# Performance work log

Hardware: AMD Instinct MI355X
Metric: run time of the kernel (lower is better)

## Reference

```python
import jax, jax.numpy as jnp
import numpy as np

GROUPS = 32
EPS = 1e-6

def groupnorm(x, gamma, beta):
    b, c, h, w = x.shape
    xg = x.reshape(b, GROUPS, c // GROUPS, h, w)
    mu = xg.mean(axis=(2, 3, 4), keepdims=True)
    var = xg.var(axis=(2, 3, 4), keepdims=True)
    xn = ((xg - mu) / jnp.sqrt(var + EPS)).reshape(b, c, h, w)
    return xn * gamma[None, :, None, None] + beta[None, :, None, None]

def conv1x1(x, w, b):
    return jnp.einsum('oc,bchw->bohw', w, x) + b[None, :, None, None]

def attn_branch(xn, wq, bq, wk, bk, v_flat, scale):
    q = conv1x1(xn, wq, bq)
    k = conv1x1(xn, wk, bk)
    b_, c, h, w = q.shape
    qf = q.reshape(b_, c, h * w)   # b c n
    kf = k.reshape(b_, c, h * w)   # b c n
    scores = jnp.einsum('bci,bcj->bij', qf, kf) * scale  # b n n
    attn = jax.nn.softmax(scores, axis=2)
    out = jnp.einsum('bcj,bij->bci', v_flat, attn)       # b c n
    return out.reshape(b_, c, h, w)

def setup_inputs() -> dict:
    key = jax.random.key(0)
    ks = jax.random.split(key, 14)
    B, C, H, W = 4, 64, 64, 64
    R = C // 16  # SE reduction
    s = 0.05
    return {
        'x1': jax.random.normal(ks[0], (B, C, H, W), jnp.float32),
        'x2': jax.random.normal(ks[1], (B, C, H, W), jnp.float32),
        'se_w1': jax.random.normal(ks[2], (R, C), jnp.float32) * s,
        'se_w2': jax.random.normal(ks[3], (C, R), jnp.float32) * s,
        'gn_gamma': jnp.ones((C,), jnp.float32),
        'gn_beta': jnp.zeros((C,), jnp.float32),
        'wq': jax.random.normal(ks[4], (C, C), jnp.float32) * s,
        'bq': jnp.zeros((C,), jnp.float32),
        'wk': jax.random.normal(ks[5], (C, C), jnp.float32) * s,
        'bk': jnp.zeros((C,), jnp.float32),
        'wv': jax.random.normal(ks[6], (C, C), jnp.float32) * s,
        'bv': jnp.zeros((C,), jnp.float32),
    }

def reference(x1, x2, se_w1, se_w2, gn_gamma, gn_beta, wq, bq, wk, bk, wv, bv):
    x = x1 + x2
    # SE channel attention (ends in sigmoid), then an EXTRA sigmoid as in source
    y = x.mean(axis=(2, 3))                         # b c
    y = jax.nn.relu(y @ se_w1.T)                    # b r
    y = jax.nn.sigmoid(y @ se_w2.T)                 # b c
    se = x * y[:, :, None, None]
    ch_w = jax.nn.sigmoid(se)
    xn = groupnorm(x, gn_gamma, gn_beta)
    v = conv1x1(xn, wv, bv)
    b_, c, h, w = v.shape
    v_flat = v.reshape(b_, c, h * w)
    scale = 1.0 / jnp.sqrt(jnp.float32(c))
    # source reuses q1/k1 convs for BOTH branches
    h1 = attn_branch(groupnorm(x1, gn_gamma, gn_beta), wq, bq, wk, bk, v_flat, scale)
    h2 = attn_branch(groupnorm(x2, gn_gamma, gn_beta), wq, bq, wk, bk, v_flat, scale)
    return 2.0 * h1 * ch_w + 2.0 * h2 * (1.0 - ch_w)
```

## Files before the change

kernel.cpp:

```cpp
#include <hip/hip_runtime.h>

#define STATS_OFF 0
#define AD_OFF    20480
#define SEY_OFF   26624
#define WQB_OFF   32768
#define WKB_OFF   40960
#define WVB_OFF   49152
#define Q_OFF     57344
#define K_OFF     (Q_OFF + 4194304)
#define V_OFF     (K_OFF + 4194304)
#define PO_OFF    (V_OFF + 2097152)

#define QSCALE 0.18033688f
#define SWZ(r) ((((r) & 7) << 3) ^ (((r) & 8) << 1))

typedef __attribute__((ext_vector_type(8))) short  short8;
typedef __attribute__((ext_vector_type(4))) short  s16x4;
typedef __attribute__((ext_vector_type(2))) unsigned int u32x2;
typedef __attribute__((ext_vector_type(4))) float  f32x4;

#if __has_builtin(__builtin_amdgcn_exp2f)
__device__ inline float fexp2(float x) { return __builtin_amdgcn_exp2f(x); }
#else
__device__ inline float fexp2(float x) { return exp2f(x); }
#endif

__device__ inline ushort f2b(float f) {
  return (ushort)((__float_as_uint(f) + 0x8000u) >> 16);
}
__device__ inline unsigned pack2(float x, float y) {
  unsigned ux = __float_as_uint(x) + 0x8000u;
  unsigned uy = __float_as_uint(y) + 0x8000u;
  return __builtin_amdgcn_perm(uy, ux, 0x07060302);
}
__device__ inline float b2f(ushort u) { return __uint_as_float(((unsigned)u) << 16); }

__device__ inline f32x4 mfma16(short8 a, short8 b, f32x4 c) {
  return __builtin_amdgcn_mfma_f32_16x16x32_bf16(a, b, c, 0, 0, 0);
}

__device__ inline float wsum64(float v) {
  #pragma unroll
  for (int o = 32; o > 0; o >>= 1) v += __shfl_down(v, o, 64);
  return v;
}

__global__ __launch_bounds__(256) void sc_stats(const float* __restrict__ x1,
                                                const float* __restrict__ x2,
                                                float* __restrict__ stats,
                                                const float* __restrict__ wq,
                                                const float* __restrict__ wk,
                                                const float* __restrict__ wv,
                                                ushort* __restrict__ wqb,
                                                ushort* __restrict__ wkb,
                                                ushort* __restrict__ wvb) {
  int blk = blockIdx.x;
  int bc = blk >> 2, chunk = blk & 3;
  const float4* p1 = (const float4*)(x1 + (size_t)bc * 4096 + chunk * 1024);
  const float4* p2 = (const float4*)(x2 + (size_t)bc * 4096 + chunk * 1024);
  float4 a = p1[threadIdx.x], b = p2[threadIdx.x];
  float s1 = a.x + a.y + a.z + a.w;
  float q1 = a.x*a.x + a.y*a.y + a.z*a.z + a.w*a.w;
  float s2 = b.x + b.y + b.z + b.w;
  float q2 = b.x*b.x + b.y*b.y + b.z*b.z + b.w*b.w;
  float p12 = a.x*b.x + a.y*b.y + a.z*b.z + a.w*b.w;
  s1 = wsum64(s1); q1 = wsum64(q1); s2 = wsum64(s2); q2 = wsum64(q2); p12 = wsum64(p12);
  __shared__ float red[4][5];
  int w = threadIdx.x >> 6, ln = threadIdx.x & 63;
  if (ln == 0) { red[w][0] = s1; red[w][1] = q1; red[w][2] = s2; red[w][3] = q2; red[w][4] = p12; }
  __syncthreads();
  if (threadIdx.x < 5) {
    float acc = 0;
    #pragma unroll
    for (int ww = 0; ww < 4; ww++) acc += red[ww][threadIdx.x];
    stats[(size_t)blk * 5 + threadIdx.x] = acc;
  }
  if (blk >= 976) {
    int idx = (blk - 976) * 256 + threadIdx.x;
    int arr = idx >> 12, e = idx & 4095;
    if (arr == 0)      wqb[e] = f2b(wq[e] * QSCALE);
    else if (arr == 1) wkb[e] = f2b(wk[e]);
    else               wvb[e] = f2b(wv[e]);
  }
}

__global__ __launch_bounds__(256) void sc_prep(const float* __restrict__ stats,
                                               const float* __restrict__ w1,
                                               const float* __restrict__ w2,
                                               const float* __restrict__ gamma,
                                               const float* __restrict__ beta,
                                               float* __restrict__ ad, float* __restrict__ sey) {
  int t = threadIdx.x; int b = t >> 6, c = t & 63;
  float s1 = 0, q1 = 0, s2 = 0, q2 = 0, p12 = 0;
  #pragma unroll
  for (int ch = 0; ch < 4; ch++) {
    const float* sp = stats + (size_t)(t * 4 + ch) * 5;
    s1 += sp[0]; q1 += sp[1]; s2 += sp[2]; q2 += sp[3]; p12 += sp[4];
  }
  float sx = s1 + s2, qx = q1 + q2 + 2.f * p12;
  __shared__ float smu[256], sS[3][256], sQ[3][256], sy[16];
  smu[t] = sx * (1.f / 4096.f);
  sS[0][t] = sx; sQ[0][t] = qx; sS[1][t] = s1; sQ[1][t] = q1; sS[2][t] = s2; sQ[2][t] = q2;
  __syncthreads();
  if (t < 16) {
    int bb = t >> 2, r = t & 3; float acc = 0.f;
    for (int cc = 0; cc < 64; cc++) acc += w1[r*64+cc] * smu[bb*64+cc];
    sy[t] = fmaxf(acc, 0.f);
  }
  __syncthreads();
  float acc = 0.f;
  #pragma unroll
  for (int r = 0; r < 4; r++) acc += w2[c*4+r] * sy[b*4+r];
  sey[t] = 1.f / (1.f + fexp2(-acc * 1.44269504f));
  int prt = t ^ 1;
  float g = gamma[c], bt = beta[c];
  #pragma unroll
  for (int s = 0; s < 3; s++) {
    float S = sS[s][t] + sS[s][prt], Q = sQ[s][t] + sQ[s][prt];
    float mean = S * (1.f / 8192.f);
    float var  = Q * (1.f / 8192.f) - mean * mean;
    float rstd = rsqrtf(var + 1e-6f);
    float a = g * rstd;
    ad[((s*256) + t)*2 + 0] = a;
    ad[((s*256) + t)*2 + 1] = bt - mean * a;
  }
}

__global__ __launch_bounds__(256) void sc_proj(const float* __restrict__ x1, const float* __restrict__ x2,
    const float* __restrict__ ad,
    const float* __restrict__ wq, const float* __restrict__ bq,
    const float* __restrict__ wk, const float* __restrict__ bk,
    const float* __restrict__ wv, const float* __restrict__ bv,
    const ushort* __restrict__ wqb, const ushort* __restrict__ wkb, const ushort* __restrict__ wvb,
    ushort* __restrict__ qout, ushort* __restrict__ kout, ushort* __restrict__ vout) {
  int pt = blockIdx.x, src = blockIdx.y, b = blockIdx.z, t = threadIdx.x;
  __shared__ ushort xlds[64 * 66];
  __shared__ ushort olds[64 * 66];
  __shared__ float sd[64], sbias[2][64];
  if (t < 64) sd[t] = ad[((src*256) + b*64 + t)*2 + 1];
  __syncthreads();
  {
    int c = t >> 2, pq = (t & 3) * 16;
    const float* px1 = x1 + ((size_t)(b*64 + c))*4096 + pt*64 + pq;
    const float* px2 = x2 + ((size_t)(b*64 + c))*4096 + pt*64 + pq;
    float av = ad[((src*256) + b*64 + c)*2 + 0];
    #pragma unroll
    for (int k4 = 0; k4 < 4; k4++) {
      float4 v1 = *(const float4*)(px1 + 4*k4);
      float xv[4];
      if (src == 1) { xv[0]=v1.x; xv[1]=v1.y; xv[2]=v1.z; xv[3]=v1.w; }
      else {
        float4 v2 = *(const float4*)(px2 + 4*k4);
        if (src == 2) { xv[0]=v2.x; xv[1]=v2.y; xv[2]=v2.z; xv[3]=v2.w; }
        else { xv[0]=v1.x+v2.x; xv[1]=v1.y+v2.y; xv[2]=v1.z+v2.z; xv[3]=v1.w+v2.w; }
      }
      #pragma unroll
      for (int k = 0; k < 4; k++)
        xlds[(pq + 4*k4 + k)*66 + c] = f2b(av * xv[k]);
    }
  }
  int nbias = (src == 0) ? 64 : 128;
  if (t < nbias) {
    int proj = t >> 6, o = t & 63;
    const float* W  = (src == 0) ? wv : (proj == 0 ? wq : wk);
    const float* bs = (src == 0) ? bv : (proj == 0 ? bq : bk);
    float acc = bs[o];
    for (int cc = 0; cc < 64; cc++) acc += W[o*64+cc] * sd[cc];
    if (src != 0 && proj == 0) acc *= QSCALE;
    sbias[proj][o] = acc;
  }
  __syncthreads();
  int wave = t >> 6, lane = t & 63, quad = lane >> 4, l15 = lane & 15;
  int orow = t >> 2, ocol = (t & 3) * 16;
  if (src == 0) {
    const ushort* ap = wvb + (wave*16 + l15)*64 + quad*8;
    short8 a0 = *(const short8*)ap;
    short8 a1 = *(const short8*)(ap + 32);
    f32x4 cinit;
    #pragma unroll
    for (int r = 0; r < 4; r++) cinit[r] = sbias[0][wave*16 + quad*4 + r];
    #pragma unroll
    for (int s = 0; s < 4; s++) {
      const ushort* bp = xlds + (s*16 + l15)*66 + quad*8;
      short8 b0 = *(const short8*)bp;
      short8 b1 = *(const short8*)(bp + 32);
      f32x4 acc = mfma16(a0, b0, cinit);
      acc = mfma16(a1, b1, acc);
      #pragma unroll
      for (int r = 0; r < 4; r++)
        olds[(wave*16 + quad*4 + r)*66 + s*16 + l15] = f2b(acc[r]);
    }
    __syncthreads();
    uint4 w0 = *(const uint4*)&olds[orow*66 + ocol];
    uint4 w1 = *(const uint4*)&olds[orow*66 + ocol + 8];
    ushort* dst = vout + ((size_t)(b*64 + orow))*4096 + pt*64 + ocol;
    *(uint4*)dst = w0; *(uint4*)(dst + 8) = w1;
  } else {
    int bh = b*2 + (src - 1);
    const ushort* ap = xlds + (wave*16 + l15)*66 + quad*8;
    short8 a0 = *(const short8*)ap;
    short8 a1 = *(const short8*)(ap + 32);
    #pragma unroll
    for (int proj = 0; proj < 2; proj++) {
      const ushort* Wb = proj == 0 ? wqb : wkb;
      ushort* dst = proj == 0 ? qout : kout;
      #pragma unroll
      for (int s = 0; s < 4; s++) {
        const ushort* bp = Wb + (s*16 + l15)*64 + quad*8;
        short8 b0 = *(const short8*)bp;
        short8 b1 = *(const short8*)(bp + 32);
        float bb = sbias[proj][s*16 + l15];
        f32x4 acc = {bb, bb, bb, bb};
        acc = mfma16(a0, b0, acc);
        acc = mfma16(a1, b1, acc);
        #pragma unroll
        for (int r = 0; r < 4; r++)
          olds[(wave*16 + quad*4 + r)*66 + s*16 + l15] = f2b(acc[r]);
      }
      __syncthreads();
      uint4 w0 = *(const uint4*)&olds[orow*66 + ocol];
      uint4 w1 = *(const uint4*)&olds[orow*66 + ocol + 8];
      ushort* dp = dst + ((size_t)bh*4096 + pt*64 + orow)*64 + ocol;
      *(uint4*)dp = w0; *(uint4*)(dp + 8) = w1;
      if (proj == 0) __syncthreads();
    }
  }
}

__global__ __launch_bounds__(256, 2) void sc_flash(const ushort* __restrict__ qg,
                                                   const ushort* __restrict__ kg,
                                                   const ushort* __restrict__ vg,
                                                   ushort* __restrict__ po,
                                                   float* __restrict__ pl,
                                                   int jsbits) {
  int blk = blockIdx.x;
  int bh = blk & 7, rest = blk >> 3;
  int njs = 1 << jsbits, njt = 64 >> jsbits;
  int js = rest & (njs - 1), itile = rest >> jsbits;
  int jbase = js * (njt << 6);
  int b = bh >> 1;
  int t = threadIdx.x, wave = t >> 6, lane = t & 63, quad = lane >> 4, l15 = lane & 15;
  int i0 = itile * 256 + wave * 64;

  __shared__ ushort Klds[64 * 64];
  __shared__ ushort Vlds[64 * 64];

  short8 Qb[4][2];
  #pragma unroll
  for (int ib = 0; ib < 4; ib++) {
    const ushort* qp = qg + ((size_t)bh * 4096 + i0 + ib * 16 + l15) * 64 + quad * 8;
    Qb[ib][0] = *(const short8*)qp;
    Qb[ib][1] = *(const short8*)(qp + 32);
  }

  f32x4 O[4][4]; const f32x4 zero4 = {0.f, 0.f, 0.f, 0.f};
  #pragma unroll
  for (int ib = 0; ib < 4; ib++)
    #pragma unroll
    for (int cb = 0; cb < 4; cb++) O[ib][cb] = zero4;
  float lsum[4] = {0.f, 0.f, 0.f, 0.f};

  int sr = t >> 2, sc = (t & 3) * 16;
  int swzs = SWZ(sr);
  int swzl = SWZ(l15);
  const ushort* ksrc = kg + ((size_t)bh * 4096 + jbase + sr) * 64 + sc;
  const ushort* vsrc = vg + ((size_t)(b * 64 + sr)) * 4096 + jbase + sc;
  ushort* kd0 = Klds + sr * 64 + (sc ^ swzs);
  ushort* kd1 = Klds + sr * 64 + ((sc + 8) ^ swzs);
  ushort* vd0 = Vlds + sr * 64 + (sc ^ swzs);
  ushort* vd1 = Vlds + sr * 64 + ((sc + 8) ^ swzs);

  uint4 kr0 = *(const uint4*)ksrc, kr1 = *(const uint4*)(ksrc + 8);
  uint4 vr0 = *(const uint4*)vsrc, vr1 = *(const uint4*)(vsrc + 8);
  ksrc += 4096; vsrc += 64;

  #pragma unroll 1
  for (int jt = 0; jt < njt; jt++) {
    __syncthreads();
    *(uint4*)kd0 = kr0; *(uint4*)kd1 = kr1;
    *(uint4*)vd0 = vr0; *(uint4*)vd1 = vr1;
    __syncthreads();
    if (jt + 1 < njt) {
      kr0 = *(const uint4*)ksrc; kr1 = *(const uint4*)(ksrc + 8);
      vr0 = *(const uint4*)vsrc; vr1 = *(const uint4*)(vsrc + 8);
      ksrc += 4096; vsrc += 64;
    }

    #pragma unroll
    for (int s = 0; s < 4; s++) {
      int rowK = (s * 16 + l15) * 64;
      short8 ka0 = *(const short8*)&Klds[rowK + ((quad * 8) ^ swzl)];
      short8 ka1 = *(const short8*)&Klds[rowK + ((quad * 8 + 32) ^ swzl)];
      f32x4 S[4];
      #pragma unroll
      for (int ib = 0; ib < 4; ib++) {
        f32x4 acc = mfma16(ka0, Qb[ib][0], zero4);
        S[ib] = mfma16(ka1, Qb[ib][1], acc);
      }
      s16x4 vbf[4];
      #pragma unroll
      for (int cb = 0; cb < 4; cb++)
        vbf[cb] = *(const s16x4*)&Vlds[(cb * 16 + l15) * 64 + ((s * 16 + quad * 4) ^ swzl)];
      #pragma unroll
      for (int ib = 0; ib < 4; ib++) {
        float p0 = fexp2(S[ib][0]);
        float p1 = fexp2(S[ib][1]);
        float p2 = fexp2(S[ib][2]);
        float p3 = fexp2(S[ib][3]);
        lsum[ib] += (p0 + p1) + (p2 + p3);
        u32x2 wpk = {pack2(p0, p1), pack2(p2, p3)};
        s16x4 Pb = __builtin_bit_cast(s16x4, wpk);
        #pragma unroll
        for (int cb = 0; cb < 4; cb++)
          O[ib][cb] = __builtin_amdgcn_mfma_f32_16x16x16bf16_1k(Pb, vbf[cb], O[ib][cb], 0, 0, 0);
      }
    }
  }

  size_t slice = (size_t)(bh * njs + js) * 4096;
  #pragma unroll
  for (int ib = 0; ib < 4; ib++) {
    float lv = lsum[ib];
    lv += __shfl_xor(lv, 16, 64);
    lv += __shfl_xor(lv, 32, 64);
    if (quad == 0) pl[slice + i0 + ib * 16 + l15] = lv;
    #pragma unroll
    for (int cb = 0; cb < 4; cb++)
      #pragma unroll
      for (int r = 0; r < 4; r++)
        po[(slice + i0 + ib * 16 + quad * 4 + r) * 64 + cb * 16 + l15] = f2b(O[ib][cb][r]);
  }
}

__global__ __launch_bounds__(256) void sc_combine(const float* __restrict__ x1, const float* __restrict__ x2,
                                                  const ushort* __restrict__ po, const float* __restrict__ pl,
                                                  const float* __restrict__ sey,
                                                  float* __restrict__ out, int jsbits) {
  int njs = 1 << jsbits;
  int itile = blockIdx.x, b = blockIdx.y, ch = blockIdx.z, t = threadIdx.x;
  __shared__ float hl[2][32 * 65];
  #pragma unroll
  for (int head = 0; head < 2; head++) {
    int bh = b * 2 + head;
    int i = t >> 2, c8 = (t & 3) * 8;
    float sum[8];
    #pragma unroll
    for (int k = 0; k < 8; k++) sum[k] = 0.f;
    float lacc = 0.f;
    for (int js = 0; js < njs; js++) {
      size_t base = ((size_t)(bh * njs + js)) * 4096;
      uint4 u = *(const uint4*)(po + base * 64 + (size_t)(itile * 64 + i) * 64 + ch * 32 + c8);
      const ushort* us = (const ushort*)&u;
      #pragma unroll
      for (int k = 0; k < 8; k++) sum[k] += b2f(us[k]);
      lacc += pl[base + itile * 64 + i];
    }
    float inv = 1.f / lacc;
    #pragma unroll
    for (int k = 0; k < 8; k++) hl[head][(c8 + k) * 65 + i] = sum[k] * inv;
  }
  __syncthreads();
  #pragma unroll
  for (int it = 0; it < 8; it++) {
    int idx = it * 256 + t;
    int cl = idx >> 6, p = idx & 63;
    int c = ch * 32 + cl;
    size_t gi = ((size_t)(b * 64 + c)) * 4096 + itile * 64 + p;
    float xv = x1[gi] + x2[gi];
    float sig = 1.f / (1.f + fexp2(-xv * sey[b * 64 + c] * 1.44269504f));
    float h1 = hl[0][cl * 65 + p], h2 = hl[1][cl * 65 + p];
    out[gi] = 2.f * (h1 * sig + h2 * (1.f - sig));
  }
}

extern "C" void kernel_launch(void* const* d_in, const int* in_sizes, int n_in,
                              void* d_out, int out_size, void* d_ws, size_t ws_size,
                              hipStream_t stream) {
  (void)in_sizes; (void)n_in; (void)out_size;
  const float* x1    = (const float*)d_in[0];
  const float* x2    = (const float*)d_in[1];
  const float* se_w1 = (const float*)d_in[2];
  const float* se_w2 = (const float*)d_in[3];
  const float* gamma = (const float*)d_in[4];
  const float* beta  = (const float*)d_in[5];
  const float* wq    = (const float*)d_in[6];
  const float* bq    = (const float*)d_in[7];
  const float* wk    = (const float*)d_in[8];
  const float* bk    = (const float*)d_in[9];
  const float* wv    = (const float*)d_in[10];
  const float* bv    = (const float*)d_in[11];
  float* out = (float*)d_out;
  char* ws = (char*)d_ws;
  float*  stats = (float*)(ws + STATS_OFF);
  float*  ad    = (float*)(ws + AD_OFF);
  float*  sey   = (float*)(ws + SEY_OFF);
  ushort* wqb   = (ushort*)(ws + WQB_OFF);
  ushort* wkb   = (ushort*)(ws + WKB_OFF);
  ushort* wvb   = (ushort*)(ws + WVB_OFF);
  ushort* qb    = (ushort*)(ws + Q_OFF);
  ushort* kb    = (ushort*)(ws + K_OFF);
  ushort* vb    = (ushort*)(ws + V_OFF);

  int jsbits = 1;
  for (int jb = 3; jb >= 2; jb--) {
    size_t need = (size_t)PO_OFF + ((size_t)8 * 4096 * 64 * 2 + (size_t)8 * 4096 * 4) * (1u << jb);
    if (ws_size >= need) { jsbits = jb; break; }
  }
  int njs = 1 << jsbits;
  ushort* pob = (ushort*)(ws + PO_OFF);
  float*  plb = (float*)(ws + PO_OFF + (size_t)8 * njs * 4096 * 64 * 2);

  sc_stats  <<<1024, 256, 0, stream>>>(x1, x2, stats, wq, wk, wv, wqb, wkb, wvb);
  sc_prep   <<<1, 256, 0, stream>>>(stats, se_w1, se_w2, gamma, beta, ad, sey);
  sc_proj   <<<dim3(64, 3, 4), 256, 0, stream>>>(x1, x2, ad,
                                                 wq, bq, wk, bk, wv, bv,
                                                 wqb, wkb, wvb, qb, kb, vb);
  sc_flash  <<<8 * 16 * njs, 256, 0, stream>>>(qb, kb, vb, pob, plb, jsbits);
  sc_combine<<<dim3(64, 4, 2), 256, 0, stream>>>(x1, x2, pob, plb, sey, out, jsbits);
}
```

Baseline: 151.7 us.

## Fuse prep into stats via last-block atomic; shrink flash blocks to two waves

The single-block prep kernel is folded into the stats kernel: each block bumps a global counter after a threadfence, and the last block to arrive computes the SE gate and the groupnorm affine coefficients. This removes one kernel launch but adds a memset and an atomic. Separately, the flash attention kernel now uses 128-thread blocks covering 128 query rows, launches twice as many blocks, and sets launch bounds to 3 blocks per CU. Each thread now loads 4 uint4 chunks of K and V per tile instead of 2. The smaller blocks give more parallelism and better occupancy, at the cost of staging each K/V tile into LDS twice as often per query row.

```diff
diff --git a/kernel.cpp b/kernel.cpp
--- a/kernel.cpp
+++ b/kernel.cpp
@@ -3,6 +3,7 @@
 #define STATS_OFF 0
 #define AD_OFF    20480
 #define SEY_OFF   26624
+#define CNT_OFF   28672
 #define WQB_OFF   32768
 #define WKB_OFF   40960
 #define WVB_OFF   49152
@@ -53,12 +54,19 @@
                                                 const float* __restrict__ wv,
                                                 ushort* __restrict__ wqb,
                                                 ushort* __restrict__ wkb,
-                                                ushort* __restrict__ wvb) {
-  int blk = blockIdx.x;
+                                                ushort* __restrict__ wvb,
+                                                const float* __restrict__ w1,
+                                                const float* __restrict__ w2,
+                                                const float* __restrict__ gamma,
+                                                const float* __restrict__ beta,
+                                                float* __restrict__ ad,
+                                                float* __restrict__ sey,
+                                                int* __restrict__ cnt) {
+  int blk = blockIdx.x, t = threadIdx.x;
   int bc = blk >> 2, chunk = blk & 3;
   const float4* p1 = (const float4*)(x1 + (size_t)bc * 4096 + chunk * 1024);
   const float4* p2 = (const float4*)(x2 + (size_t)bc * 4096 + chunk * 1024);
-  float4 a = p1[threadIdx.x], b = p2[threadIdx.x];
+  float4 a = p1[t], b = p2[t];
   float s1 = a.x + a.y + a.z + a.w;
   float q1 = a.x*a.x + a.y*a.y + a.z*a.z + a.w*a.w;
   float s2 = b.x + b.y + b.z + b.w;
@@ -66,63 +74,63 @@
   float p12 = a.x*b.x + a.y*b.y + a.z*b.z + a.w*b.w;
   s1 = wsum64(s1); q1 = wsum64(q1); s2 = wsum64(s2); q2 = wsum64(q2); p12 = wsum64(p12);
   __shared__ float red[4][5];
-  int w = threadIdx.x >> 6, ln = threadIdx.x & 63;
+  int w = t >> 6, ln = t & 63;
   if (ln == 0) { red[w][0] = s1; red[w][1] = q1; red[w][2] = s2; red[w][3] = q2; red[w][4] = p12; }
   __syncthreads();
-  if (threadIdx.x < 5) {
+  if (t < 5) {
     float acc = 0;
     #pragma unroll
-    for (int ww = 0; ww < 4; ww++) acc += red[ww][threadIdx.x];
-    stats[(size_t)blk * 5 + threadIdx.x] = acc;
+    for (int ww = 0; ww < 4; ww++) acc += red[ww][t];
+    stats[(size_t)blk * 5 + t] = acc;
   }
   if (blk >= 976) {
-    int idx = (blk - 976) * 256 + threadIdx.x;
+    int idx = (blk - 976) * 256 + t;
     int arr = idx >> 12, e = idx & 4095;
     if (arr == 0)      wqb[e] = f2b(wq[e] * QSCALE);
     else if (arr == 1) wkb[e] = f2b(wk[e]);
     else               wvb[e] = f2b(wv[e]);
   }
-}
-
-__global__ __launch_bounds__(256) void sc_prep(const float* __restrict__ stats,
-                                               const float* __restrict__ w1,
-                                               const float* __restrict__ w2,
-                                               const float* __restrict__ gamma,
-                                               const float* __restrict__ beta,
-                                               float* __restrict__ ad, float* __restrict__ sey) {
-  int t = threadIdx.x; int b = t >> 6, c = t & 63;
-  float s1 = 0, q1 = 0, s2 = 0, q2 = 0, p12 = 0;
-  #pragma unroll
-  for (int ch = 0; ch < 4; ch++) {
-    const float* sp = stats + (size_t)(t * 4 + ch) * 5;
-    s1 += sp[0]; q1 += sp[1]; s2 += sp[2]; q2 += sp[3]; p12 += sp[4];
-  }
-  float sx = s1 + s2, qx = q1 + q2 + 2.f * p12;
-  __shared__ float smu[256], sS[3][256], sQ[3][256], sy[16];
-  smu[t] = sx * (1.f / 4096.f);
-  sS[0][t] = sx; sQ[0][t] = qx; sS[1][t] = s1; sQ[1][t] = q1; sS[2][t] = s2; sQ[2][t] = q2;
+  __threadfence();
+  __shared__ int lastFlag;
+  if (t == 0) lastFlag = (atomicAdd(cnt, 1) == 1023) ? 1 : 0;
   __syncthreads();
-  if (t < 16) {
-    int bb = t >> 2, r = t & 3; float acc = 0.f;
-    for (int cc = 0; cc < 64; cc++) acc += w1[r*64+cc] * smu[bb*64+cc];
-    sy[t] = fmaxf(acc, 0.f);
-  }
-  __syncthreads();
-  float acc = 0.f;
-  #pragma unroll
-  for (int r = 0; r < 4; r++) acc += w2[c*4+r] * sy[b*4+r];
-  sey[t] = 1.f / (1.f + fexp2(-acc * 1.44269504f));
-  int prt = t ^ 1;
-  float g = gamma[c], bt = beta[c];
-  #pragma unroll
-  for (int s = 0; s < 3; s++) {
-    float S = sS[s][t] + sS[s][prt], Q = sQ[s][t] + sQ[s][prt];
-    float mean = S * (1.f / 8192.f);
-    float var  = Q * (1.f / 8192.f) - mean * mean;
-    float rstd = rsqrtf(var + 1e-6f);
-    float a = g * rstd;
-    ad[((s*256) + t)*2 + 0] = a;
-    ad[((s*256) + t)*2 + 1] = bt - mean * a;
+  if (!lastFlag) return;
+  __threadfence();
+  {
+    __shared__ float smu[256], sS[3][256], sQ[3][256], sy[16];
+    int bb = t >> 6, c = t & 63;
+    float t1 = 0, t2 = 0, t3 = 0, t4 = 0, t5 = 0;
+    #pragma unroll
+    for (int ch = 0; ch < 4; ch++) {
+      const float* sp = stats + (size_t)(t * 4 + ch) * 5;
+      t1 += sp[0]; t2 += sp[1]; t3 += sp[2]; t4 += sp[3]; t5 += sp[4];
+    }
+    float sx = t1 + t3, qx = t2 + t4 + 2.f * t5;
+    smu[t] = sx * (1.f / 4096.f);
+    sS[0][t] = sx; sQ[0][t] = qx; sS[1][t] = t1; sQ[1][t] = t2; sS[2][t] = t3; sQ[2][t] = t4;
+    __syncthreads();
+    if (t < 16) {
+      int b2_ = t >> 2, r = t & 3; float acc = 0.f;
+      for (int cc = 0; cc < 64; cc++) acc += w1[r*64+cc] * smu[b2_*64+cc];
+      sy[t] = fmaxf(acc, 0.f);
+    }
+    __syncthreads();
+    float acc = 0.f;
+    #pragma unroll
+    for (int r = 0; r < 4; r++) acc += w2[c*4+r] * sy[bb*4+r];
+    sey[t] = 1.f / (1.f + fexp2(-acc * 1.44269504f));
+    int prt = t ^ 1;
+    float g = gamma[c], bt = beta[c];
+    #pragma unroll
+    for (int s = 0; s < 3; s++) {
+      float S = sS[s][t] + sS[s][prt], Q = sQ[s][t] + sQ[s][prt];
+      float mean = S * (1.f / 8192.f);
+      float var  = Q * (1.f / 8192.f) - mean * mean;
+      float rstd = rsqrtf(var + 1e-6f);
+      float av = g * rstd;
+      ad[((s*256) + t)*2 + 0] = av;
+      ad[((s*256) + t)*2 + 1] = bt - mean * av;
+    }
   }
 }
 
@@ -227,7 +235,7 @@
   }
 }
 
-__global__ __launch_bounds__(256, 2) void sc_flash(const ushort* __restrict__ qg,
+__global__ __launch_bounds__(128, 3) void sc_flash(const ushort* __restrict__ qg,
                                                    const ushort* __restrict__ kg,
                                                    const ushort* __restrict__ vg,
                                                    ushort* __restrict__ po,
@@ -240,7 +248,7 @@
   int jbase = js * (njt << 6);
   int b = bh >> 1;
   int t = threadIdx.x, wave = t >> 6, lane = t & 63, quad = lane >> 4, l15 = lane & 15;
-  int i0 = itile * 256 + wave * 64;
+  int i0 = itile * 128 + wave * 64;
 
   __shared__ ushort Klds[64 * 64];
   __shared__ ushort Vlds[64 * 64];
@@ -260,29 +268,31 @@
     for (int cb = 0; cb < 4; cb++) O[ib][cb] = zero4;
   float lsum[4] = {0.f, 0.f, 0.f, 0.f};
 
-  int sr = t >> 2, sc = (t & 3) * 16;
+  int sr = t >> 1, sc = (t & 1) * 32;
   int swzs = SWZ(sr);
   int swzl = SWZ(l15);
   const ushort* ksrc = kg + ((size_t)bh * 4096 + jbase + sr) * 64 + sc;
   const ushort* vsrc = vg + ((size_t)(b * 64 + sr)) * 4096 + jbase + sc;
-  ushort* kd0 = Klds + sr * 64 + (sc ^ swzs);
-  ushort* kd1 = Klds + sr * 64 + ((sc + 8) ^ swzs);
-  ushort* vd0 = Vlds + sr * 64 + (sc ^ swzs);
-  ushort* vd1 = Vlds + sr * 64 + ((sc + 8) ^ swzs);
-
-  uint4 kr0 = *(const uint4*)ksrc, kr1 = *(const uint4*)(ksrc + 8);
-  uint4 vr0 = *(const uint4*)vsrc, vr1 = *(const uint4*)(vsrc + 8);
+  ushort* kbase = Klds + sr * 64;
+  ushort* vbase = Vlds + sr * 64;
+
+  uint4 kr[4], vr[4];
+  #pragma unroll
+  for (int m = 0; m < 4; m++) { kr[m] = *(const uint4*)(ksrc + 8*m); vr[m] = *(const uint4*)(vsrc + 8*m); }
   ksrc += 4096; vsrc += 64;
 
   #pragma unroll 1
   for (int jt = 0; jt < njt; jt++) {
     __syncthreads();
-    *(uint4*)kd0 = kr0; *(uint4*)kd1 = kr1;
-    *(uint4*)vd0 = vr0; *(uint4*)vd1 = vr1;
+    #pragma unroll
+    for (int m = 0; m < 4; m++) {
+      *(uint4*)(kbase + ((sc + 8*m) ^ swzs)) = kr[m];
+      *(uint4*)(vbase + ((sc + 8*m) ^ swzs)) = vr[m];
+    }
     __syncthreads();
     if (jt + 1 < njt) {
-      kr0 = *(const uint4*)ksrc; kr1 = *(const uint4*)(ksrc + 8);
-      vr0 = *(const uint4*)vsrc; vr1 = *(const uint4*)(vsrc + 8);
+      #pragma unroll
+      for (int m = 0; m < 4; m++) { kr[m] = *(const uint4*)(ksrc + 8*m); vr[m] = *(const uint4*)(vsrc + 8*m); }
       ksrc += 4096; vsrc += 64;
     }
 
@@ -394,6 +404,7 @@
   float*  stats = (float*)(ws + STATS_OFF);
   float*  ad    = (float*)(ws + AD_OFF);
   float*  sey   = (float*)(ws + SEY_OFF);
+  int*    cnt   = (int*)(ws + CNT_OFF);
   ushort* wqb   = (ushort*)(ws + WQB_OFF);
   ushort* wkb   = (ushort*)(ws + WKB_OFF);
   ushort* wvb   = (ushort*)(ws + WVB_OFF);
@@ -410,11 +421,12 @@
   ushort* pob = (ushort*)(ws + PO_OFF);
   float*  plb = (float*)(ws + PO_OFF + (size_t)8 * njs * 4096 * 64 * 2);
 
-  sc_stats  <<<1024, 256, 0, stream>>>(x1, x2, stats, wq, wk, wv, wqb, wkb, wvb);
-  sc_prep   <<<1, 256, 0, stream>>>(stats, se_w1, se_w2, gamma, beta, ad, sey);
+  hipMemsetAsync(cnt, 0, sizeof(int), stream);
+  sc_stats  <<<1024, 256, 0, stream>>>(x1, x2, stats, wq, wk, wv, wqb, wkb, wvb,
+                                       se_w1, se_w2, gamma, beta, ad, sey, cnt);
   sc_proj   <<<dim3(64, 3, 4), 256, 0, stream>>>(x1, x2, ad,
                                                  wq, bq, wk, bk, wv, bv,
                                                  wqb, wkb, wvb, qb, kb, vb);
-  sc_flash  <<<8 * 16 * njs, 256, 0, stream>>>(qb, kb, vb, pob, plb, jsbits);
+  sc_flash  <<<8 * 32 * njs, 128, 0, stream>>>(qb, kb, vb, pob, plb, jsbits);
   sc_combine<<<dim3(64, 4, 2), 256, 0, stream>>>(x1, x2, pob, plb, sey, out, jsbits);
 }
```

After: 387.2 us. 2.55x slower.

## Fuse split-K combine into flash kernel via last-block atomic counter

Applied to the files above, without the earlier changes.

Drops the separate combine kernel. Each flash block increments a per-(batch, i-tile) counter after writing its partial output, and the last arriving block reduces the partials across heads and j-splits, then applies the sigmoid gate and writes the final output. The counter is reset in the prep kernel. This removes one kernel launch and its tail, but the epilogue runs on a single block per 256-row tile, which serialises the combine work onto fewer blocks and adds fence and atomic overhead.

```diff
diff --git a/kernel.cpp b/kernel.cpp
--- a/kernel.cpp
+++ b/kernel.cpp
@@ -3,6 +3,7 @@
 #define STATS_OFF 0
 #define AD_OFF    20480
 #define SEY_OFF   26624
+#define CCNT_OFF  28672
 #define WQB_OFF   32768
 #define WKB_OFF   40960
 #define WVB_OFF   49152
@@ -54,11 +55,11 @@
                                                 ushort* __restrict__ wqb,
                                                 ushort* __restrict__ wkb,
                                                 ushort* __restrict__ wvb) {
-  int blk = blockIdx.x;
+  int blk = blockIdx.x, t = threadIdx.x;
   int bc = blk >> 2, chunk = blk & 3;
   const float4* p1 = (const float4*)(x1 + (size_t)bc * 4096 + chunk * 1024);
   const float4* p2 = (const float4*)(x2 + (size_t)bc * 4096 + chunk * 1024);
-  float4 a = p1[threadIdx.x], b = p2[threadIdx.x];
+  float4 a = p1[t], b = p2[t];
   float s1 = a.x + a.y + a.z + a.w;
   float q1 = a.x*a.x + a.y*a.y + a.z*a.z + a.w*a.w;
   float s2 = b.x + b.y + b.z + b.w;
@@ -66,17 +67,17 @@
   float p12 = a.x*b.x + a.y*b.y + a.z*b.z + a.w*b.w;
   s1 = wsum64(s1); q1 = wsum64(q1); s2 = wsum64(s2); q2 = wsum64(q2); p12 = wsum64(p12);
   __shared__ float red[4][5];
-  int w = threadIdx.x >> 6, ln = threadIdx.x & 63;
+  int w = t >> 6, ln = t & 63;
   if (ln == 0) { red[w][0] = s1; red[w][1] = q1; red[w][2] = s2; red[w][3] = q2; red[w][4] = p12; }
   __syncthreads();
-  if (threadIdx.x < 5) {
+  if (t < 5) {
     float acc = 0;
     #pragma unroll
-    for (int ww = 0; ww < 4; ww++) acc += red[ww][threadIdx.x];
-    stats[(size_t)blk * 5 + threadIdx.x] = acc;
+    for (int ww = 0; ww < 4; ww++) acc += red[ww][t];
+    stats[(size_t)blk * 5 + t] = acc;
   }
   if (blk >= 976) {
-    int idx = (blk - 976) * 256 + threadIdx.x;
+    int idx = (blk - 976) * 256 + t;
     int arr = idx >> 12, e = idx & 4095;
     if (arr == 0)      wqb[e] = f2b(wq[e] * QSCALE);
     else if (arr == 1) wkb[e] = f2b(wk[e]);
@@ -89,8 +90,10 @@
                                                const float* __restrict__ w2,
                                                const float* __restrict__ gamma,
                                                const float* __restrict__ beta,
-                                               float* __restrict__ ad, float* __restrict__ sey) {
+                                               float* __restrict__ ad, float* __restrict__ sey,
+                                               int* __restrict__ ccnt) {
   int t = threadIdx.x; int b = t >> 6, c = t & 63;
+  if (t < 64) ccnt[t] = 0;
   float s1 = 0, q1 = 0, s2 = 0, q2 = 0, p12 = 0;
   #pragma unroll
   for (int ch = 0; ch < 4; ch++) {
@@ -230,8 +233,13 @@
 __global__ __launch_bounds__(256, 2) void sc_flash(const ushort* __restrict__ qg,
                                                    const ushort* __restrict__ kg,
                                                    const ushort* __restrict__ vg,
+                                                   const float* __restrict__ x1,
+                                                   const float* __restrict__ x2,
+                                                   const float* __restrict__ sey,
                                                    ushort* __restrict__ po,
                                                    float* __restrict__ pl,
+                                                   int* __restrict__ ccnt,
+                                                   float* __restrict__ out,
                                                    int jsbits) {
   int blk = blockIdx.x;
   int bh = blk & 7, rest = blk >> 3;
@@ -242,8 +250,9 @@
   int t = threadIdx.x, wave = t >> 6, lane = t & 63, quad = lane >> 4, l15 = lane & 15;
   int i0 = itile * 256 + wave * 64;
 
-  __shared__ ushort Klds[64 * 64];
-  __shared__ ushort Vlds[64 * 64];
+  __shared__ __align__(16) char smem[16640];
+  ushort* Klds = (ushort*)smem;
+  ushort* Vlds = (ushort*)(smem + 8192);
 
   short8 Qb[4][2];
   #pragma unroll
@@ -330,46 +339,51 @@
       for (int r = 0; r < 4; r++)
         po[(slice + i0 + ib * 16 + quad * 4 + r) * 64 + cb * 16 + l15] = f2b(O[ib][cb][r]);
   }
-}
-
-__global__ __launch_bounds__(256) void sc_combine(const float* __restrict__ x1, const float* __restrict__ x2,
-                                                  const ushort* __restrict__ po, const float* __restrict__ pl,
-                                                  const float* __restrict__ sey,
-                                                  float* __restrict__ out, int jsbits) {
-  int njs = 1 << jsbits;
-  int itile = blockIdx.x, b = blockIdx.y, ch = blockIdx.z, t = threadIdx.x;
-  __shared__ float hl[2][32 * 65];
-  #pragma unroll
-  for (int head = 0; head < 2; head++) {
-    int bh = b * 2 + head;
-    int i = t >> 2, c8 = (t & 3) * 8;
-    float sum[8];
-    #pragma unroll
-    for (int k = 0; k < 8; k++) sum[k] = 0.f;
-    float lacc = 0.f;
-    for (int js = 0; js < njs; js++) {
-      size_t base = ((size_t)(bh * njs + js)) * 4096;
-      uint4 u = *(const uint4*)(po + base * 64 + (size_t)(itile * 64 + i) * 64 + ch * 32 + c8);
-      const ushort* us = (const ushort*)&u;
-      #pragma unroll
-      for (int k = 0; k < 8; k++) sum[k] += b2f(us[k]);
-      lacc += pl[base + itile * 64 + i];
-    }
-    float inv = 1.f / lacc;
-    #pragma unroll
-    for (int k = 0; k < 8; k++) hl[head][(c8 + k) * 65 + i] = sum[k] * inv;
-  }
-  __syncthreads();
-  #pragma unroll
-  for (int it = 0; it < 8; it++) {
-    int idx = it * 256 + t;
-    int cl = idx >> 6, p = idx & 63;
-    int c = ch * 32 + cl;
-    size_t gi = ((size_t)(b * 64 + c)) * 4096 + itile * 64 + p;
-    float xv = x1[gi] + x2[gi];
-    float sig = 1.f / (1.f + fexp2(-xv * sey[b * 64 + c] * 1.44269504f));
-    float h1 = hl[0][cl * 65 + p], h2 = hl[1][cl * 65 + p];
-    out[gi] = 2.f * (h1 * sig + h2 * (1.f - sig));
+
+  __threadfence();
+  __shared__ int lastFlag;
+  if (t == 0) lastFlag = (atomicAdd(&ccnt[b * 16 + itile], 1) == 2 * njs - 1) ? 1 : 0;
+  __syncthreads();
+  if (!lastFlag) return;
+  __threadfence();
+  float (*hl)[32 * 65] = (float (*)[32 * 65])smem;
+  for (int sub = 0; sub < 4; sub++) {
+    int it64 = itile * 4 + sub;
+    for (int ch = 0; ch < 2; ch++) {
+      __syncthreads();
+      #pragma unroll
+      for (int head = 0; head < 2; head++) {
+        int bh2 = b * 2 + head;
+        int i = t >> 2, c8 = (t & 3) * 8;
+        float sum[8];
+        #pragma unroll
+        for (int k = 0; k < 8; k++) sum[k] = 0.f;
+        float lacc = 0.f;
+        for (int js2 = 0; js2 < njs; js2++) {
+          size_t base = ((size_t)(bh2 * njs + js2)) * 4096;
+          uint4 u = *(const uint4*)(po + base * 64 + (size_t)(it64 * 64 + i) * 64 + ch * 32 + c8);
+          const ushort* us = (const ushort*)&u;
+          #pragma unroll
+          for (int k = 0; k < 8; k++) sum[k] += b2f(us[k]);
+          lacc += pl[base + it64 * 64 + i];
+        }
+        float inv = 1.f / lacc;
+        #pragma unroll
+        for (int k = 0; k < 8; k++) hl[head][(c8 + k) * 65 + i] = sum[k] * inv;
+      }
+      __syncthreads();
+      #pragma unroll
+      for (int it = 0; it < 8; it++) {
+        int idx = it * 256 + t;
+        int cl = idx >> 6, p = idx & 63;
+        int c = ch * 32 + cl;
+        size_t gi = ((size_t)(b * 64 + c)) * 4096 + it64 * 64 + p;
+        float xv = x1[gi] + x2[gi];
+        float sig = 1.f / (1.f + fexp2(-xv * sey[b * 64 + c] * 1.44269504f));
+        float h1 = hl[0][cl * 65 + p], h2 = hl[1][cl * 65 + p];
+        out[gi] = 2.f * (h1 * sig + h2 * (1.f - sig));
+      }
+    }
   }
 }
 
@@ -394,6 +408,7 @@
   float*  stats = (float*)(ws + STATS_OFF);
   float*  ad    = (float*)(ws + AD_OFF);
   float*  sey   = (float*)(ws + SEY_OFF);
+  int*    ccnt  = (int*)(ws + CCNT_OFF);
   ushort* wqb   = (ushort*)(ws + WQB_OFF);
   ushort* wkb   = (ushort*)(ws + WKB_OFF);
   ushort* wvb   = (ushort*)(ws + WVB_OFF);
@@ -410,11 +425,11 @@
   ushort* pob = (ushort*)(ws + PO_OFF);
   float*  plb = (float*)(ws + PO_OFF + (size_t)8 * njs * 4096 * 64 * 2);
 
-  sc_stats  <<<1024, 256, 0, stream>>>(x1, x2, stats, wq, wk, wv, wqb, wkb, wvb);
-  sc_prep   <<<1, 256, 0, stream>>>(stats, se_w1, se_w2, gamma, beta, ad, sey);
-  sc_proj   <<<dim3(64, 3, 4), 256, 0, stream>>>(x1, x2, ad,
-                                                 wq, bq, wk, bk, wv, bv,
-                                                 wqb, wkb, wvb, qb, kb, vb);
-  sc_flash  <<<8 * 16 * njs, 256, 0, stream>>>(qb, kb, vb, pob, plb, jsbits);
-  sc_combine<<<dim3(64, 4, 2), 256, 0, stream>>>(x1, x2, pob, plb, sey, out, jsbits);
-}
+  sc_stats <<<1024, 256, 0, stream>>>(x1, x2, stats, wq, wk, wv, wqb, wkb, wvb);
+  sc_prep  <<<1, 256, 0, stream>>>(stats, se_w1, se_w2, gamma, beta, ad, sey, ccnt);
+  sc_proj  <<<dim3(64, 3, 4), 256, 0, stream>>>(x1, x2, ad,
+                                                wq, bq, wk, bk, wv, bv,
+                                                wqb, wkb, wvb, qb, kb, vb);
+  sc_flash <<<8 * 16 * njs, 256, 0, stream>>>(qb, kb, vb, x1, x2, sey,
+                                              pob, plb, ccnt, out, jsbits);
+}
```

New measurement: 346.7 us. 2.29x slower.
